# Performance work log

Measured on AMD Instinct MI355X. Metric: run time of the kernel, lower is better.

## Reference

```python
import jax, jax.numpy as jnp
import numpy as np

B, T, C = 2, 2048, 1024
H = 16
HD = C // H  # head_size = 64
FF = 4 * C
EPS = 1e-5


def layernorm(x, g, b):
    mu = jnp.mean(x, axis=-1, keepdims=True)
    var = jnp.mean(jnp.square(x - mu), axis=-1, keepdims=True)
    return (x - mu) * jax.lax.rsqrt(var + EPS) * g + b


def setup_inputs() -> dict:
    key = jax.random.key(0)
    ks = jax.random.split(key, 12)
    s_c = 1.0 / np.sqrt(C)
    s_hc = 1.0 / np.sqrt(C)
    s_ff = 1.0 / np.sqrt(FF)
    return {
        "x": jax.random.normal(ks[0], (B, T, C), jnp.float32),
        "Wq": jax.random.normal(ks[1], (H, C, HD), jnp.float32) * s_hc,
        "Wk": jax.random.normal(ks[2], (H, C, HD), jnp.float32) * s_hc,
        "Wv": jax.random.normal(ks[3], (H, C, HD), jnp.float32) * s_hc,
        "Wo": jax.random.normal(ks[4], (C, C), jnp.float32) * s_c,
        "bo": jax.random.normal(ks[5], (C,), jnp.float32) * 0.01,
        "W1": jax.random.normal(ks[6], (C, FF), jnp.float32) * s_c,
        "b1": jax.random.normal(ks[7], (FF,), jnp.float32) * 0.01,
        "W2": jax.random.normal(ks[8], (FF, C), jnp.float32) * s_ff,
        "b2": jax.random.normal(ks[9], (C,), jnp.float32) * 0.01,
        "g1": jnp.ones((C,), jnp.float32),
        "be1": jnp.zeros((C,), jnp.float32),
        "g2": jnp.ones((C,), jnp.float32),
        "be2": jnp.zeros((C,), jnp.float32),
    }


def reference(x, Wq, Wk, Wv, Wo, bo, W1, b1, W2, b2, g1, be1, g2, be2):
    # --- self-attention sublayer (pre-LN, residual) ---
    h = layernorm(x, g1, be1)                               # [B,T,C]
    q = jnp.einsum("btc,hcd->bhtd", h, Wq)                   # [B,H,T,HD]
    k = jnp.einsum("btc,hcd->bhtd", h, Wk)
    v = jnp.einsum("btc,hcd->bhtd", h, Wv)
    scores = jnp.einsum("bhtd,bhsd->bhts", q, k) * (HD ** -0.5)
    causal = jnp.tril(jnp.ones((T, T), bool))
    scores = jnp.where(causal, scores, -jnp.inf)
    wei = jax.nn.softmax(scores, axis=-1)                    # [B,H,T,T]
    attn = jnp.einsum("bhts,bhsd->bhtd", wei, v)             # [B,H,T,HD]
    attn = attn.transpose(0, 2, 1, 3).reshape(B, T, H * HD)  # concat heads
    x = x + attn @ Wo + bo
    # --- feedforward sublayer (pre-LN, residual) ---
    h2 = layernorm(x, g2, be2)
    x = x + jax.nn.relu(h2 @ W1 + b1) @ W2 + b2
    return x
```

## Files before the change

kernel.cpp:

```cpp
#include <hip/hip_runtime.h>
#include <hip/hip_bf16.h>
#include <cstdint>
#include <cstddef>
#include <cstring>

#define B_ 2
#define T_ 2048
#define C_ 1024
#define H_ 16
#define HD_ 64
#define FF_ 4096
#define BT_ (B_*T_)

typedef __attribute__((ext_vector_type(8))) short short8;
typedef __attribute__((ext_vector_type(4))) float f32x4;

__device__ __forceinline__ float bf2f(ushort u) {
    return __uint_as_float(((uint)u) << 16);
}
__device__ __forceinline__ ushort f2bf(float f) {
    uint x = __float_as_uint(f);
    return (ushort)((x + 0x7fffu + ((x >> 16) & 1u)) >> 16);
}
__device__ __forceinline__ ushort f2bf_hw(float f) {
    __hip_bfloat16 h = __float2bfloat16(f);
    ushort u;
    __builtin_memcpy(&u, &h, 2);
    return u;
}

#define GLDS16(g, l)                                                        \
    __builtin_amdgcn_global_load_lds(                                       \
        (const __attribute__((address_space(1))) void*)(g),                 \
        (__attribute__((address_space(3))) void*)(l), 16, 0, 0)

__global__ __launch_bounds__(256) void prep(
    const float* __restrict__ Wq, const float* __restrict__ Wk,
    const float* __restrict__ Wv, const float* __restrict__ Wo,
    const float* __restrict__ W1, const float* __restrict__ W2,
    const float* __restrict__ x,  const float* __restrict__ g1,
    const float* __restrict__ be1,
    ushort* __restrict__ qkvw, ushort* __restrict__ Wo_t,
    ushort* __restrict__ W1_t, ushort* __restrict__ W2_t,
    ushort* __restrict__ h_bf)
{
    int fb = blockIdx.x;
    int tid = threadIdx.x;
    __shared__ float tile[32][33];
    __shared__ float ss[4], qs[4];

    if (fb >= 12288) {
        int row = fb - 12288;
        const float* xr = x + (size_t)row * C_;
        float4 v = *(const float4*)(xr + tid * 4);
        float s = v.x + v.y + v.z + v.w;
        float q = v.x*v.x + v.y*v.y + v.z*v.z + v.w*v.w;
        #pragma unroll
        for (int off = 32; off > 0; off >>= 1) {
            s += __shfl_down(s, off);
            q += __shfl_down(q, off);
        }
        if ((tid & 63) == 0) { ss[tid >> 6] = s; qs[tid >> 6] = q; }
        __syncthreads();
        s = ss[0] + ss[1] + ss[2] + ss[3];
        q = qs[0] + qs[1] + qs[2] + qs[3];
        float mu  = s * (1.0f / C_);
        float var = q * (1.0f / C_) - mu * mu;
        float r = rsqrtf(var + 1e-5f);
        float4 gv = *(const float4*)(g1 + tid * 4);
        float4 bv = *(const float4*)(be1 + tid * 4);
        ushort4 o;
        o.x = f2bf((v.x - mu) * r * gv.x + bv.x);
        o.y = f2bf((v.y - mu) * r * gv.y + bv.y);
        o.z = f2bf((v.z - mu) * r * gv.z + bv.z);
        o.w = f2bf((v.w - mu) * r * gv.w + bv.w);
        *(ushort4*)(h_bf + (size_t)row * C_ + tid * 4) = o;
        return;
    }

    const float* in;
    ushort* out;
    int Cc, ldo, bx, by;
    if (fb < 3072) {
        int z = fb >> 6;
        int rem = fb & 63;
        in = (z < 16 ? Wq : (z < 32 ? Wk : Wv)) + (size_t)(z & 15) * 65536;
        out = qkvw + (size_t)z * 65536;
        Cc = 64; ldo = 1024;
        bx = rem & 1; by = rem >> 1;
    } else if (fb < 4096) {
        int t = fb - 3072;
        in = Wo; out = Wo_t; Cc = 1024; ldo = 1024;
        bx = t & 31; by = t >> 5;
    } else if (fb < 8192) {
        int t = fb - 4096;
        in = W1; out = W1_t; Cc = 4096; ldo = 1024;
        bx = t & 127; by = t >> 7;
    } else {
        int t = fb - 8192;
        in = W2; out = W2_t; Cc = 1024; ldo = 4096;
        bx = t & 31; by = t >> 5;
    }
    int c0 = bx * 32, r0 = by * 32;
    int tx = tid & 31, ty = tid >> 5;
    #pragma unroll
    for (int i = 0; i < 4; i++) {
        int r = ty + i * 8;
        tile[r][tx] = in[(size_t)(r0 + r) * Cc + c0 + tx];
    }
    __syncthreads();
    #pragma unroll
    for (int i = 0; i < 4; i++) {
        int c = ty + i * 8;
        out[(size_t)(c0 + c) * ldo + r0 + tx] = f2bf(tile[tx][c]);
    }
}

template<int EPI, bool OUT_BF16>
__global__ __launch_bounds__(512, 4) void gemm2(
    const ushort* __restrict__ A,
    const ushort* __restrict__ Bt,
    void* __restrict__ Cout,
    const float* __restrict__ bias,
    const float* __restrict__ resid,
    int M, int N, int K, int KS)
{
    __shared__ ushort As[3][128 * 32];
    __shared__ ushort Bs[3][256 * 32];

    int gx = gridDim.x;
    int nwg = gx * gridDim.y;
    int bid = blockIdx.y * gx + blockIdx.x;
    int cpx = nwg >> 3;
    int swz = (bid & 7) * cpx + (bid >> 3);
    int bx = swz % gx, by = swz / gx;

    int tid  = threadIdx.x;
    int lane = tid & 63;
    int lr = lane & 15, lq = lane >> 4;
    int wave = tid >> 6;
    int wr = wave >> 2, wc = wave & 3;
    int m0 = by * 128, n0 = bx * 256;
    int Koff = blockIdx.z * KS;
    size_t zoff = (size_t)blockIdx.z * ((size_t)M * N);

    f32x4 acc[4][4];
    #pragma unroll
    for (int i = 0; i < 4; i++)
        #pragma unroll
        for (int j = 0; j < 4; j++)
            acc[i][j] = {0.f, 0.f, 0.f, 0.f};

    int srow = tid >> 2;
    int scol = ((tid & 3) ^ ((srow >> 1) & 3)) * 8;
    const ushort* gA  = A  + (size_t)(m0 + srow) * K + Koff + scol;
    const ushort* gB0 = Bt + (size_t)(n0 + srow) * K + Koff + scol;
    const ushort* gB1 = Bt + (size_t)(n0 + 128 + srow) * K + Koff + scol;
    int NT = KS / 32;

    auto stage = [&](int kt, int buf) {
        int off = kt * 32;
        GLDS16(gA + off,  (char*)As[buf] + wave * 1024);
        GLDS16(gB0 + off, (char*)Bs[buf] + wave * 1024);
        GLDS16(gB1 + off, (char*)Bs[buf] + 8192 + wave * 1024);
    };

    stage(0, 0);
    stage(1, 1);
    asm volatile("s_waitcnt vmcnt(3)" ::: "memory");
    __builtin_amdgcn_s_barrier();

    int so = (lq ^ ((lr >> 1) & 3)) << 4;

    int cur = 0;
    for (int t = 0; t < NT; ++t) {
        const char* Ab = (const char*)As[cur] + (wr * 64 + lr) * 64 + so;
        const char* Bb = (const char*)Bs[cur] + (wc * 64 + lr) * 64 + so;

        short8 a[4], b[4];
        #pragma unroll
        for (int fr = 0; fr < 4; fr++)
            a[fr] = *(const short8*)(Ab + fr * 1024);
        #pragma unroll
        for (int fc = 0; fc < 4; fc++)
            b[fc] = *(const short8*)(Bb + fc * 1024);

        if (t + 2 < NT) {
            int nb = cur + 2;
            if (nb >= 3) nb -= 3;
            stage(t + 2, nb);
        }

        #pragma unroll
        for (int fr = 0; fr < 4; fr++)
            #pragma unroll
            for (int fc = 0; fc < 4; fc++)
                acc[fr][fc] = __builtin_amdgcn_mfma_f32_16x16x32_bf16(
                    a[fr], b[fc], acc[fr][fc], 0, 0, 0);

        if (t + 1 == NT) break;
        if (t + 2 < NT)
            asm volatile("s_waitcnt vmcnt(3)" ::: "memory");
        else
            asm volatile("s_waitcnt vmcnt(0)" ::: "memory");
        __builtin_amdgcn_s_barrier();
        cur = (cur == 2) ? 0 : cur + 1;
    }

    #pragma unroll
    for (int fr = 0; fr < 4; fr++) {
        #pragma unroll
        for (int fc = 0; fc < 4; fc++) {
            int col = n0 + wc * 64 + fc * 16 + lr;
            #pragma unroll
            for (int j = 0; j < 4; j++) {
                int row = m0 + wr * 64 + fr * 16 + lq * 4 + j;
                float v = acc[fr][fc][j];
                if (EPI & 1) v += bias[col];
                if (EPI & 2) v = fmaxf(v, 0.f);
                if (EPI & 4) v += resid[(size_t)row * N + col];
                if (OUT_BF16)
                    ((ushort*)Cout)[zoff + (size_t)row * N + col] = f2bf(v);
                else
                    ((float*)Cout)[zoff + (size_t)row * N + col] = v;
            }
        }
    }
}

__global__ __launch_bounds__(512, 4) void gemm_qkvt(
    const ushort* __restrict__ h_bf,
    const ushort* __restrict__ qkvw,
    ushort* __restrict__ qk_act,
    ushort* __restrict__ vt)
{
    __shared__ ushort As[3][128 * 32];
    __shared__ ushort Bs[3][256 * 32];

    const ushort* A; const ushort* Bt; ushort* Cb;
    int N, gx, nwg, bid;
    int fb = blockIdx.x;
    if (fb < 256) {
        A = h_bf; Bt = qkvw; Cb = qk_act;
        N = 2048; gx = 8; nwg = 256; bid = fb;
    } else {
        A = qkvw + (size_t)2 * 1024 * 1024; Bt = h_bf; Cb = vt;
        N = BT_; gx = 16; nwg = 128; bid = fb - 256;
    }
    const int K = C_;
    int cpx = nwg >> 3;
    int swz = (bid & 7) * cpx + (bid >> 3);
    int bx = swz % gx, by = swz / gx;

    int tid  = threadIdx.x;
    int lane = tid & 63;
    int lr = lane & 15, lq = lane >> 4;
    int wave = tid >> 6;
    int wr = wave >> 2, wc = wave & 3;
    int m0 = by * 128, n0 = bx * 256;

    f32x4 acc[4][4];
    #pragma unroll
    for (int i = 0; i < 4; i++)
        #pragma unroll
        for (int j = 0; j < 4; j++)
            acc[i][j] = {0.f, 0.f, 0.f, 0.f};

    int srow = tid >> 2;
    int scol = ((tid & 3) ^ ((srow >> 1) & 3)) * 8;
    const ushort* gA  = A  + (size_t)(m0 + srow) * K + scol;
    const ushort* gB0 = Bt + (size_t)(n0 + srow) * K + scol;
    const ushort* gB1 = Bt + (size_t)(n0 + 128 + srow) * K + scol;
    const int NT = 32;

    auto stage = [&](int kt, int buf) {
        int off = kt * 32;
        GLDS16(gA + off,  (char*)As[buf] + wave * 1024);
        GLDS16(gB0 + off, (char*)Bs[buf] + wave * 1024);
        GLDS16(gB1 + off, (char*)Bs[buf] + 8192 + wave * 1024);
    };

    stage(0, 0);
    stage(1, 1);
    asm volatile("s_waitcnt vmcnt(3)" ::: "memory");
    __builtin_amdgcn_s_barrier();

    int so = (lq ^ ((lr >> 1) & 3)) << 4;

    int cur = 0;
    for (int t = 0; t < NT; ++t) {
        const char* Ab = (const char*)As[cur] + (wr * 64 + lr) * 64 + so;
        const char* Bb = (const char*)Bs[cur] + (wc * 64 + lr) * 64 + so;

        short8 a[4], b[4];
        #pragma unroll
        for (int fr = 0; fr < 4; fr++)
            a[fr] = *(const short8*)(Ab + fr * 1024);
        #pragma unroll
        for (int fc = 0; fc < 4; fc++)
            b[fc] = *(const short8*)(Bb + fc * 1024);

        if (t + 2 < NT) {
            int nb = cur + 2;
            if (nb >= 3) nb -= 3;
            stage(t + 2, nb);
        }

        #pragma unroll
        for (int fr = 0; fr < 4; fr++)
            #pragma unroll
            for (int fc = 0; fc < 4; fc++)
                acc[fr][fc] = __builtin_amdgcn_mfma_f32_16x16x32_bf16(
                    a[fr], b[fc], acc[fr][fc], 0, 0, 0);

        if (t + 1 == NT) break;
        if (t + 2 < NT)
            asm volatile("s_waitcnt vmcnt(3)" ::: "memory");
        else
            asm volatile("s_waitcnt vmcnt(0)" ::: "memory");
        __builtin_amdgcn_s_barrier();
        cur = (cur == 2) ? 0 : cur + 1;
    }

    #pragma unroll
    for (int fr = 0; fr < 4; fr++) {
        #pragma unroll
        for (int fc = 0; fc < 4; fc++) {
            int col = n0 + wc * 64 + fc * 16 + lr;
            #pragma unroll
            for (int j = 0; j < 4; j++) {
                int row = m0 + wr * 64 + fr * 16 + lq * 4 + j;
                Cb[(size_t)row * N + col] = f2bf(acc[fr][fc][j]);
            }
        }
    }
}

__global__ __launch_bounds__(256) void wo_ln(float* __restrict__ out,
                                             ushort* __restrict__ h,
                                             const ushort* __restrict__ p,
                                             const float* __restrict__ bo,
                                             const float* __restrict__ x,
                                             const float* __restrict__ g,
                                             const float* __restrict__ be) {
    int row = blockIdx.x;
    int tid = threadIdx.x;
    size_t base = (size_t)row * C_ + tid * 4;
    float4 v = *(const float4*)(x + base);
    float4 c = *(const float4*)(bo + tid * 4);
    #pragma unroll
    for (int z = 0; z < 4; z++) {
        ushort4 a = *(const ushort4*)(p + (size_t)z * BT_ * C_ + base);
        v.x += bf2f(a.x); v.y += bf2f(a.y);
        v.z += bf2f(a.z); v.w += bf2f(a.w);
    }
    v.x += c.x; v.y += c.y; v.z += c.z; v.w += c.w;
    *(float4*)(out + base) = v;

    float s = v.x + v.y + v.z + v.w;
    float q = v.x*v.x + v.y*v.y + v.z*v.z + v.w*v.w;
    #pragma unroll
    for (int off = 32; off > 0; off >>= 1) {
        s += __shfl_down(s, off);
        q += __shfl_down(q, off);
    }
    __shared__ float ss[4], qs[4];
    if ((tid & 63) == 0) { ss[tid >> 6] = s; qs[tid >> 6] = q; }
    __syncthreads();
    s = ss[0] + ss[1] + ss[2] + ss[3];
    q = qs[0] + qs[1] + qs[2] + qs[3];
    float mu  = s * (1.0f / C_);
    float var = q * (1.0f / C_) - mu * mu;
    float r = rsqrtf(var + 1e-5f);
    float4 gv = *(const float4*)(g + tid * 4);
    float4 bv = *(const float4*)(be + tid * 4);
    ushort4 o;
    o.x = f2bf((v.x - mu) * r * gv.x + bv.x);
    o.y = f2bf((v.y - mu) * r * gv.y + bv.y);
    o.z = f2bf((v.z - mu) * r * gv.z + bv.z);
    o.w = f2bf((v.w - mu) * r * gv.w + bv.w);
    *(ushort4*)(h + base) = o;
}

__global__ __launch_bounds__(256) void ff2_red4(float* __restrict__ out,
                                                const ushort* __restrict__ p,
                                                const float* __restrict__ b2) {
    size_t i = (size_t)blockIdx.x * 256 + threadIdx.x;
    float4 o = ((float4*)out)[i];
    float4 c = ((const float4*)b2)[i & 255];
    #pragma unroll
    for (int z = 0; z < 4; z++) {
        ushort4 a = ((const ushort4*)(p + (size_t)z * BT_ * C_))[i];
        o.x += bf2f(a.x); o.y += bf2f(a.y);
        o.z += bf2f(a.z); o.w += bf2f(a.w);
    }
    o.x += c.x; o.y += c.y; o.z += c.z; o.w += c.w;
    ((float4*)out)[i] = o;
}

__global__ __launch_bounds__(256, 3) void attn_mfma(const ushort* __restrict__ qk,
                                                    const ushort* __restrict__ vt,
                                                    ushort* __restrict__ Opart,
                                                    float* __restrict__ ml) {
    const float C2 = 0.18033688011f;
    const float THR2 = 12.0f;

    int flat = blockIdx.x;
    int xcd = flat & 7;
    int idx = flat >> 3;
    int bh  = xcd * 4 + (idx & 3);
    int qz  = idx >> 2;
    int qa  = 15 - (qz >> 1);
    int z   = qz & 1;

    int bb = bh >> 4;
    int head = bh & 15;
    int q0 = qa * 128;

    int tid  = threadIdx.x;
    int lane = tid & 63;
    int lr = lane & 15, lq = lane >> 4;
    int wave = tid >> 6;
    int qw = q0 + wave * 32;

    __shared__ ushort Ks[2][64 * 64];
    __shared__ ushort Vs[2][64 * 64];
    __shared__ ushort Ps[4][32 * 64];
    char* pw = (char*)Ps[wave];

    short8 qf[2][2];
    {
        const ushort* qb = qk + ((size_t)(bb * T_ + qw)) * 2048 + head * 64;
        #pragma unroll
        for (int mt = 0; mt < 2; mt++)
            #pragma unroll
            for (int kk = 0; kk < 2; kk++)
                qf[mt][kk] = *(const short8*)(qb + (size_t)(mt*16 + lr) * 2048 + kk*32 + lq*8);
    }

    f32x4 acc[2][4];
    f32x4 lsum[2];
    float m2[2][4];
    #pragma unroll
    for (int mt = 0; mt < 2; mt++) {
        #pragma unroll
        for (int dt = 0; dt < 4; dt++) acc[mt][dt] = {0.f, 0.f, 0.f, 0.f};
        lsum[mt] = {0.f, 0.f, 0.f, 0.f};
        #pragma unroll
        for (int j = 0; j < 4; j++) m2[mt][j] = -INFINITY;
    }

    const short8 onesf = {(short)0x3F80, (short)0x3F80, (short)0x3F80, (short)0x3F80,
                          (short)0x3F80, (short)0x3F80, (short)0x3F80, (short)0x3F80};

    int srow = tid >> 3;
    int ssc = ((tid & 7) ^ (srow & 7)) * 8;
    const ushort* kg0 = qk + ((size_t)(bb * T_ + srow)) * 2048 + 1024 + head * 64 + ssc;
    const ushort* vg0 = vt + ((size_t)(head * 64 + srow)) * 4096 + (size_t)bb * 2048 + ssc;

    auto stage = [&](int it, int buf) {
        int s0 = it * 64;
        char* Kb = (char*)Ks[buf] + wave * 1024;
        char* Vb = (char*)Vs[buf] + wave * 1024;
        GLDS16(kg0 + (size_t)s0 * 2048,        Kb);
        GLDS16(kg0 + (size_t)(s0 + 32) * 2048, Kb + 4096);
        GLDS16(vg0 + s0,                        Vb);
        GLDS16(vg0 + (size_t)32 * 4096 + s0,    Vb + 4096);
    };

    int nt = 2 * (qa + 1);
    stage(z, 0);
    __syncthreads();
    int cur = 0;

    for (int it = z; it < nt; it += 2) {
        if (it + 2 < nt) stage(it + 2, cur ^ 1);

        int s0h = it * 64;
        if (s0h <= qw + 31) {
            const ushort* Kc = Ks[cur];
            const ushort* Vc = Vs[cur];

            f32x4 sa[2][4];
            __builtin_amdgcn_s_setprio(1);
            #pragma unroll
            for (int n = 0; n < 4; n++) {
                int row = n*16 + lr;
                const char* kbase = (const char*)Kc + row*128;
                short8 kf0 = *(const short8*)(kbase + ((lq       ^ (row & 7)) << 4));
                short8 kf1 = *(const short8*)(kbase + (((4 + lq) ^ (row & 7)) << 4));
                #pragma unroll
                for (int mt = 0; mt < 2; mt++) {
                    f32x4 tq = {0.f, 0.f, 0.f, 0.f};
                    tq = __builtin_amdgcn_mfma_f32_16x16x32_bf16(qf[mt][0], kf0, tq, 0, 0, 0);
                    tq = __builtin_amdgcn_mfma_f32_16x16x32_bf16(qf[mt][1], kf1, tq, 0, 0, 0);
                    sa[mt][n] = tq;
                }
            }
            __builtin_amdgcn_s_setprio(0);

            if (s0h + 63 > qw) {
                #pragma unroll
                for (int mt = 0; mt < 2; mt++)
                    #pragma unroll
                    for (int n = 0; n < 4; n++)
                        #pragma unroll
                        for (int j = 0; j < 4; j++) {
                            int scolm = s0h + n*16 + lr;
                            int qrow = qw + mt*16 + lq*4 + j;
                            if (scolm > qrow) sa[mt][n][j] = -INFINITY;
                        }
            }

            float vmax2[2][4];
            bool growf = false;
            #pragma unroll
            for (int mt = 0; mt < 2; mt++) {
                #pragma unroll
                for (int j = 0; j < 4; j++) {
                    float v = fmaxf(fmaxf(sa[mt][0][j], sa[mt][1][j]),
                                    fmaxf(sa[mt][2][j], sa[mt][3][j]));
                    #pragma unroll
                    for (int off = 1; off < 16; off <<= 1)
                        v = fmaxf(v, __shfl_xor(v, off));
                    float v2 = v * C2;
                    vmax2[mt][j] = v2;
                    growf |= (v2 > m2[mt][j] + THR2);
                }
            }
            if (__any(growf)) {
                #pragma unroll
                for (int mt = 0; mt < 2; mt++)
                    #pragma unroll
                    for (int j = 0; j < 4; j++) {
                        float m2n = fmaxf(m2[mt][j], vmax2[mt][j]);
                        float corr = __builtin_amdgcn_exp2f(m2[mt][j] - m2n);
                        m2[mt][j] = m2n;
                        lsum[mt][j] *= corr;
                        #pragma unroll
                        for (int dt = 0; dt < 4; dt++)
                            acc[mt][dt][j] *= corr;
                    }
            }

            #pragma unroll
            for (int mt = 0; mt < 2; mt++)
                #pragma unroll
                for (int n = 0; n < 4; n++)
                    #pragma unroll
                    for (int j = 0; j < 4; j++) {
                        float p = __builtin_amdgcn_exp2f(
                            fmaf(sa[mt][n][j], C2, -m2[mt][j]));
                        int row = mt*16 + lq*4 + j;
                        int col = n*16 + lr;
                        int byte = row*128 + ((((col >> 3) ^ (row & 7))) << 4) + (col & 7)*2;
                        *(ushort*)(pw + byte) = f2bf_hw(p);
                    }

            short8 pf[2][2];
            #pragma unroll
            for (int mt = 0; mt < 2; mt++) {
                int row = mt*16 + lr;
                #pragma unroll
                for (int kk = 0; kk < 2; kk++)
                    pf[mt][kk] = *(const short8*)(pw + row*128
                                   + (((kk*4 + lq) ^ (row & 7)) << 4));
            }
            __builtin_amdgcn_s_setprio(1);
            #pragma unroll
            for (int kk = 0; kk < 2; kk++)
                #pragma unroll
                for (int mt = 0; mt < 2; mt++)
                    lsum[mt] = __builtin_amdgcn_mfma_f32_16x16x32_bf16(
                        pf[mt][kk], onesf, lsum[mt], 0, 0, 0);
            #pragma unroll
            for (int dt = 0; dt < 4; dt++) {
                int row = dt*16 + lr;
                const char* vbase = (const char*)Vc + row*128;
                #pragma unroll
                for (int kk = 0; kk < 2; kk++) {
                    short8 vf = *(const short8*)(vbase
                                  + (((kk*4 + lq) ^ (row & 7)) << 4));
                    #pragma unroll
                    for (int mt = 0; mt < 2; mt++)
                        acc[mt][dt] = __builtin_amdgcn_mfma_f32_16x16x32_bf16(
                            pf[mt][kk], vf, acc[mt][dt], 0, 0, 0);
                }
            }
            __builtin_amdgcn_s_setprio(0);
        }

        __syncthreads();
        cur ^= 1;
    }

    ushort* ob = Opart + (size_t)z * ((size_t)BT_ * C_)
               + ((size_t)(bb * T_ + qw)) * 1024 + head * 64;
    #pragma unroll
    for (int mt = 0; mt < 2; mt++)
        #pragma unroll
        for (int j = 0; j < 4; j++) {
            float l = lsum[mt][j];
            float inv = l > 0.f ? 1.0f / l : 0.f;
            #pragma unroll
            for (int dt = 0; dt < 4; dt++)
                ob[(size_t)(mt*16 + lq*4 + j) * 1024 + dt*16 + lr] =
                    f2bf(acc[mt][dt][j] * inv);
        }
    if (lr == 0) {
        float* mlz = ml + ((size_t)(z * 16 + head)) * (BT_ * 2);
        #pragma unroll
        for (int mt = 0; mt < 2; mt++)
            #pragma unroll
            for (int j = 0; j < 4; j++) {
                size_t row = (size_t)(bb * T_ + qw + mt*16 + lq*4 + j);
                *(float2*)(mlz + row * 2) = make_float2(m2[mt][j], lsum[mt][j]);
            }
    }
}

__global__ __launch_bounds__(256) void attn_comb(const ushort* __restrict__ Opart,
                                                 const float* __restrict__ ml,
                                                 ushort* __restrict__ outb) {
    int row = blockIdx.x;
    int tid = threadIdx.x;
    int col = tid * 4;
    int head = col >> 6;
    float2 ml0 = *(const float2*)(ml + ((size_t)head * BT_ + row) * 2);
    float2 ml1 = *(const float2*)(ml + ((size_t)(16 + head) * BT_ + row) * 2);
    float m = fmaxf(ml0.x, ml1.x);
    float w0 = ml0.y * __builtin_amdgcn_exp2f(ml0.x - m);
    float w1 = ml1.y * __builtin_amdgcn_exp2f(ml1.x - m);
    float inv = 1.0f / (w0 + w1);
    w0 *= inv; w1 *= inv;
    size_t idx = (size_t)row * C_ + col;
    ushort4 a = *(const ushort4*)(Opart + idx);
    ushort4 b = *(const ushort4*)(Opart + (size_t)BT_ * C_ + idx);
    ushort4 o;
    o.x = f2bf(bf2f(a.x) * w0 + bf2f(b.x) * w1);
    o.y = f2bf(bf2f(a.y) * w0 + bf2f(b.y) * w1);
    o.z = f2bf(bf2f(a.z) * w0 + bf2f(b.z) * w1);
    o.w = f2bf(bf2f(a.w) * w0 + bf2f(b.w) * w1);
    *(ushort4*)(outb + idx) = o;
}

extern "C" void kernel_launch(void* const* d_in, const int* in_sizes, int n_in,
                              void* d_out, int out_size, void* d_ws, size_t ws_size,
                              hipStream_t stream) {
    const float* x   = (const float*)d_in[0];
    const float* Wq  = (const float*)d_in[1];
    const float* Wk  = (const float*)d_in[2];
    const float* Wv  = (const float*)d_in[3];
    const float* Wo  = (const float*)d_in[4];
    const float* bo  = (const float*)d_in[5];
    const float* W1  = (const float*)d_in[6];
    const float* b1  = (const float*)d_in[7];
    const float* W2  = (const float*)d_in[8];
    const float* b2  = (const float*)d_in[9];
    const float* g1  = (const float*)d_in[10];
    const float* be1 = (const float*)d_in[11];
    const float* g2  = (const float*)d_in[12];
    const float* be2 = (const float*)d_in[13];
    float* out = (float*)d_out;

    char* ws = (char*)d_ws;
    const size_t MB = 1 << 20;
    ushort* h_bf    = (ushort*)(ws);
    ushort* qk_act  = (ushort*)(ws + 8*MB);
    ushort* vt      = (ushort*)(ws + 24*MB);
    ushort* attn_bf = (ushort*)(ws);
    ushort* W2_t    = (ushort*)(ws + 40*MB);
    ushort* qkvw    = (ushort*)(ws + 48*MB);
    ushort* Wo_t    = (ushort*)(ws + 54*MB);
    ushort* W1_t    = (ushort*)(ws + 56*MB);
    ushort* Opart   = (ushort*)(ws + 64*MB);
    float*  mlbuf   = (float*)(ws + 80*MB);
    ushort* p_wo    = (ushort*)(ws + 8*MB);
    ushort* ff1     = (ushort*)(ws + 8*MB);
    ushort* p_ff2   = (ushort*)(ws + 48*MB);

    prep<<<dim3(16384), dim3(256), 0, stream>>>(
        Wq, Wk, Wv, Wo, W1, W2, x, g1, be1,
        qkvw, Wo_t, W1_t, W2_t, h_bf);

    gemm_qkvt<<<dim3(384), dim3(512), 0, stream>>>(h_bf, qkvw, qk_act, vt);

    attn_mfma<<<dim3(1024), dim3(256), 0, stream>>>(qk_act, vt, Opart, mlbuf);
    attn_comb<<<dim3(BT_), dim3(256), 0, stream>>>(Opart, mlbuf, attn_bf);

    gemm2<0, true><<<dim3(1024/256, BT_/128, 4), dim3(512), 0, stream>>>(
        attn_bf, Wo_t, p_wo, nullptr, nullptr, BT_, C_, C_, 256);
    wo_ln<<<dim3(BT_), dim3(256), 0, stream>>>(out, h_bf, p_wo, bo, x, g2, be2);

    gemm2<1|2, true><<<dim3(FF_/256, BT_/128, 1), dim3(512), 0, stream>>>(
        h_bf, W1_t, ff1, b1, nullptr, BT_, FF_, C_, C_);

    gemm2<0, true><<<dim3(1024/256, BT_/128, 4), dim3(512), 0, stream>>>(
        ff1, W2_t, p_ff2, nullptr, nullptr, BT_, C_, FF_, 1024);
    ff2_red4<<<dim3(BT_*C_/4/256), dim3(256), 0, stream>>>(out, p_ff2, b2);
}
```

Measured before the change: 226.1 us.

## Split P tile into two 32-column halves to shrink LDS and raise occupancy

The attention kernel now writes the softmax probabilities to LDS in two 32-key halves, each consumed right away by the PV and row-sum MFMAs, instead of staging the full 64-key tile. This halves the per-wave P scratch in shared memory, and launch bounds are raised from 3 to 4 blocks per CU. The aim is more resident waves and overlap of exp work with MFMA. The cost is tighter register limits, which may cause spills, and interleaved LDS write/read phases that add latency.

```diff
diff --git a/kernel.cpp b/kernel.cpp
--- a/kernel.cpp
+++ b/kernel.cpp
@@ -398,7 +398,7 @@
     ((float4*)out)[i] = o;
 }
 
-__global__ __launch_bounds__(256, 3) void attn_mfma(const ushort* __restrict__ qk,
+__global__ __launch_bounds__(256, 4) void attn_mfma(const ushort* __restrict__ qk,
                                                     const ushort* __restrict__ vt,
                                                     ushort* __restrict__ Opart,
                                                     float* __restrict__ ml) {
@@ -425,7 +425,7 @@
 
     __shared__ ushort Ks[2][64 * 64];
     __shared__ ushort Vs[2][64 * 64];
-    __shared__ ushort Ps[4][32 * 64];
+    __shared__ ushort Ps[4][32 * 32];
     char* pw = (char*)Ps[wave];
 
     short8 qf[2][2];
@@ -544,50 +544,47 @@
             }
 
             #pragma unroll
-            for (int mt = 0; mt < 2; mt++)
-                #pragma unroll
-                for (int n = 0; n < 4; n++)
+            for (int h2 = 0; h2 < 2; h2++) {
+                #pragma unroll
+                for (int mt = 0; mt < 2; mt++)
                     #pragma unroll
-                    for (int j = 0; j < 4; j++) {
-                        float p = __builtin_amdgcn_exp2f(
-                            fmaf(sa[mt][n][j], C2, -m2[mt][j]));
-                        int row = mt*16 + lq*4 + j;
-                        int col = n*16 + lr;
-                        int byte = row*128 + ((((col >> 3) ^ (row & 7))) << 4) + (col & 7)*2;
-                        *(ushort*)(pw + byte) = f2bf_hw(p);
-                    }
-
-            short8 pf[2][2];
-            #pragma unroll
-            for (int mt = 0; mt < 2; mt++) {
-                int row = mt*16 + lr;
-                #pragma unroll
-                for (int kk = 0; kk < 2; kk++)
-                    pf[mt][kk] = *(const short8*)(pw + row*128
-                                   + (((kk*4 + lq) ^ (row & 7)) << 4));
-            }
-            __builtin_amdgcn_s_setprio(1);
-            #pragma unroll
-            for (int kk = 0; kk < 2; kk++)
+                    for (int nn = 0; nn < 2; nn++)
+                        #pragma unroll
+                        for (int j = 0; j < 4; j++) {
+                            float p = __builtin_amdgcn_exp2f(
+                                fmaf(sa[mt][2*h2 + nn][j], C2, -m2[mt][j]));
+                            int row = mt*16 + lq*4 + j;
+                            int col32 = nn*16 + lr;
+                            int byte = row*64 + ((((col32 >> 3) ^ (row & 3))) << 4)
+                                     + (col32 & 7)*2;
+                            *(ushort*)(pw + byte) = f2bf_hw(p);
+                        }
+
+                short8 pf[2];
+                #pragma unroll
+                for (int mt = 0; mt < 2; mt++) {
+                    int row = mt*16 + lr;
+                    pf[mt] = *(const short8*)(pw + row*64
+                               + ((lq ^ (row & 3)) << 4));
+                }
+
+                __builtin_amdgcn_s_setprio(1);
                 #pragma unroll
                 for (int mt = 0; mt < 2; mt++)
                     lsum[mt] = __builtin_amdgcn_mfma_f32_16x16x32_bf16(
-                        pf[mt][kk], onesf, lsum[mt], 0, 0, 0);
-            #pragma unroll
-            for (int dt = 0; dt < 4; dt++) {
-                int row = dt*16 + lr;
-                const char* vbase = (const char*)Vc + row*128;
-                #pragma unroll
-                for (int kk = 0; kk < 2; kk++) {
-                    short8 vf = *(const short8*)(vbase
-                                  + (((kk*4 + lq) ^ (row & 7)) << 4));
+                        pf[mt], onesf, lsum[mt], 0, 0, 0);
+                #pragma unroll
+                for (int dt = 0; dt < 4; dt++) {
+                    int row = dt*16 + lr;
+                    short8 vf = *(const short8*)((const char*)Vc + row*128
+                                  + (((h2*4 + lq) ^ (row & 7)) << 4));
                     #pragma unroll
                     for (int mt = 0; mt < 2; mt++)
                         acc[mt][dt] = __builtin_amdgcn_mfma_f32_16x16x32_bf16(
-                            pf[mt][kk], vf, acc[mt][dt], 0, 0, 0);
+                            pf[mt], vf, acc[mt][dt], 0, 0, 0);
                 }
-            }
-            __builtin_amdgcn_s_setprio(0);
+                __builtin_amdgcn_s_setprio(0);
+            }
         }
 
         __syncthreads();
```

Result: slower. 232.3 us (+2.7%).

## Enlarge GEMM block tile to 256x256 with 8x4 MFMA fragments per wave

Applied to the files above, without the earlier changes.

The generic GEMM kernel's block tile grows from 128x256 to 256x256. Each wave now computes 128x64 outputs using 8x4 accumulator fragments, which doubles the A-tile shared memory and cuts global loads per FLOP. Launch bounds drop to 2 blocks per CU to leave room for the extra registers and LDS. The Wo, FF1 and FF2 GEMMs now launch half as many blocks, which risks lower occupancy and tail effects, since FF2 has only 256 blocks split over K.

```diff
diff --git a/kernel.cpp b/kernel.cpp
--- a/kernel.cpp
+++ b/kernel.cpp
@@ -117,15 +117,14 @@
 }
 
 template<int EPI, bool OUT_BF16>
-__global__ __launch_bounds__(512, 4) void gemm2(
+__global__ __launch_bounds__(512, 2) void gemm3(
     const ushort* __restrict__ A,
     const ushort* __restrict__ Bt,
     void* __restrict__ Cout,
     const float* __restrict__ bias,
-    const float* __restrict__ resid,
     int M, int N, int K, int KS)
 {
-    __shared__ ushort As[3][128 * 32];
+    __shared__ ushort As[3][256 * 32];
     __shared__ ushort Bs[3][256 * 32];
 
     int gx = gridDim.x;
@@ -139,47 +138,49 @@
     int lane = tid & 63;
     int lr = lane & 15, lq = lane >> 4;
     int wave = tid >> 6;
-    int wr = wave >> 2, wc = wave & 3;
-    int m0 = by * 128, n0 = bx * 256;
+    int wm = wave >> 2, wn = wave & 3;
+    int m0 = by * 256, n0 = bx * 256;
     int Koff = blockIdx.z * KS;
     size_t zoff = (size_t)blockIdx.z * ((size_t)M * N);
 
-    f32x4 acc[4][4];
-    #pragma unroll
-    for (int i = 0; i < 4; i++)
+    f32x4 acc[8][4];
+    #pragma unroll
+    for (int i = 0; i < 8; i++)
         #pragma unroll
         for (int j = 0; j < 4; j++)
             acc[i][j] = {0.f, 0.f, 0.f, 0.f};
 
     int srow = tid >> 2;
     int scol = ((tid & 3) ^ ((srow >> 1) & 3)) * 8;
-    const ushort* gA  = A  + (size_t)(m0 + srow) * K + Koff + scol;
+    const ushort* gA0 = A  + (size_t)(m0 + srow) * K + Koff + scol;
+    const ushort* gA1 = gA0 + (size_t)128 * K;
     const ushort* gB0 = Bt + (size_t)(n0 + srow) * K + Koff + scol;
-    const ushort* gB1 = Bt + (size_t)(n0 + 128 + srow) * K + Koff + scol;
+    const ushort* gB1 = gB0 + (size_t)128 * K;
     int NT = KS / 32;
 
     auto stage = [&](int kt, int buf) {
         int off = kt * 32;
-        GLDS16(gA + off,  (char*)As[buf] + wave * 1024);
+        GLDS16(gA0 + off, (char*)As[buf] + wave * 1024);
+        GLDS16(gA1 + off, (char*)As[buf] + 8192 + wave * 1024);
         GLDS16(gB0 + off, (char*)Bs[buf] + wave * 1024);
         GLDS16(gB1 + off, (char*)Bs[buf] + 8192 + wave * 1024);
     };
 
     stage(0, 0);
     stage(1, 1);
-    asm volatile("s_waitcnt vmcnt(3)" ::: "memory");
+    asm volatile("s_waitcnt vmcnt(4)" ::: "memory");
     __builtin_amdgcn_s_barrier();
 
     int so = (lq ^ ((lr >> 1) & 3)) << 4;
 
     int cur = 0;
     for (int t = 0; t < NT; ++t) {
-        const char* Ab = (const char*)As[cur] + (wr * 64 + lr) * 64 + so;
-        const char* Bb = (const char*)Bs[cur] + (wc * 64 + lr) * 64 + so;
-
-        short8 a[4], b[4];
-        #pragma unroll
-        for (int fr = 0; fr < 4; fr++)
+        const char* Ab = (const char*)As[cur] + (wm * 128 + lr) * 64 + so;
+        const char* Bb = (const char*)Bs[cur] + (wn * 64 + lr) * 64 + so;
+
+        short8 a[8], b[4];
+        #pragma unroll
+        for (int fr = 0; fr < 8; fr++)
             a[fr] = *(const short8*)(Ab + fr * 1024);
         #pragma unroll
         for (int fc = 0; fc < 4; fc++)
@@ -192,7 +193,7 @@
         }
 
         #pragma unroll
-        for (int fr = 0; fr < 4; fr++)
+        for (int fr = 0; fr < 8; fr++)
             #pragma unroll
             for (int fc = 0; fc < 4; fc++)
                 acc[fr][fc] = __builtin_amdgcn_mfma_f32_16x16x32_bf16(
@@ -200,7 +201,7 @@
 
         if (t + 1 == NT) break;
         if (t + 2 < NT)
-            asm volatile("s_waitcnt vmcnt(3)" ::: "memory");
+            asm volatile("s_waitcnt vmcnt(4)" ::: "memory");
         else
             asm volatile("s_waitcnt vmcnt(0)" ::: "memory");
         __builtin_amdgcn_s_barrier();
@@ -208,17 +209,16 @@
     }
 
     #pragma unroll
-    for (int fr = 0; fr < 4; fr++) {
+    for (int fr = 0; fr < 8; fr++) {
         #pragma unroll
         for (int fc = 0; fc < 4; fc++) {
-            int col = n0 + wc * 64 + fc * 16 + lr;
+            int col = n0 + wn * 64 + fc * 16 + lr;
             #pragma unroll
             for (int j = 0; j < 4; j++) {
-                int row = m0 + wr * 64 + fr * 16 + lq * 4 + j;
+                int row = m0 + wm * 128 + fr * 16 + lq * 4 + j;
                 float v = acc[fr][fc][j];
                 if (EPI & 1) v += bias[col];
                 if (EPI & 2) v = fmaxf(v, 0.f);
-                if (EPI & 4) v += resid[(size_t)row * N + col];
                 if (OUT_BF16)
                     ((ushort*)Cout)[zoff + (size_t)row * N + col] = f2bf(v);
                 else
@@ -688,14 +688,14 @@
     attn_mfma<<<dim3(1024), dim3(256), 0, stream>>>(qk_act, vt, Opart, mlbuf);
     attn_comb<<<dim3(BT_), dim3(256), 0, stream>>>(Opart, mlbuf, attn_bf);
 
-    gemm2<0, true><<<dim3(1024/256, BT_/128, 4), dim3(512), 0, stream>>>(
-        attn_bf, Wo_t, p_wo, nullptr, nullptr, BT_, C_, C_, 256);
+    gemm3<0, true><<<dim3(1024/256, BT_/256, 4), dim3(512), 0, stream>>>(
+        attn_bf, Wo_t, p_wo, nullptr, BT_, C_, C_, 256);
     wo_ln<<<dim3(BT_), dim3(256), 0, stream>>>(out, h_bf, p_wo, bo, x, g2, be2);
 
-    gemm2<1|2, true><<<dim3(FF_/256, BT_/128, 1), dim3(512), 0, stream>>>(
-        h_bf, W1_t, ff1, b1, nullptr, BT_, FF_, C_, C_);
-
-    gemm2<0, true><<<dim3(1024/256, BT_/128, 4), dim3(512), 0, stream>>>(
-        ff1, W2_t, p_ff2, nullptr, nullptr, BT_, C_, FF_, 1024);
+    gemm3<1|2, true><<<dim3(FF_/256, BT_/256, 1), dim3(512), 0, stream>>>(
+        h_bf, W1_t, ff1, b1, BT_, FF_, C_, C_);
+
+    gemm3<0, true><<<dim3(1024/256, BT_/256, 4), dim3(512), 0, stream>>>(
+        ff1, W2_t, p_ff2, nullptr, BT_, C_, FF_, 1024);
     ff2_red4<<<dim3(BT_*C_/4/256), dim3(256), 0, stream>>>(out, p_ff2, b2);
 }
```

After: 219.4 us. 1.03x faster.
